# Kernel tuning notes

Hardware: AMD Instinct MI355X
Metric: run time of the kernel (lower is better)

## Reference

```python
import jax, jax.numpy as jnp
import numpy as np

K = 8  # hardcoded knn_point(8, ...) in the original module


def setup_inputs() -> dict:
    key = jax.random.key(0)
    k1, k2, k3 = jax.random.split(key, 3)
    B, N, S, C = 8, 8192, 2048, 256
    return {
        "xyz": jax.random.normal(k1, (B, 3, N), dtype=jnp.float32),
        "sparse_xyz": jax.random.normal(k2, (B, 3, S), dtype=jnp.float32),
        "sparse_feat": jax.random.normal(k3, (B, C, S), dtype=jnp.float32),
    }


def reference(xyz, sparse_xyz, sparse_feat):
    # xyz: [B,3,N] dense query points; sparse_xyz: [B,3,S]; sparse_feat: [B,C,S]
    B, _, N = xyz.shape
    x = jnp.transpose(xyz, (0, 2, 1))          # [B,N,3]
    sx = jnp.transpose(sparse_xyz, (0, 2, 1))  # [B,S,3]
    sf = jnp.transpose(sparse_feat, (0, 2, 1)) # [B,S,C]

    sqr = (jnp.sum(x * x, axis=-1)[:, :, None]
           + jnp.sum(sx * sx, axis=-1)[:, None, :]
           - 2.0 * jnp.einsum('bnc,bsc->bns', x, sx))

    # K nearest neighbors (smallest distance) -> indices [B,N,K]
    _, idx = jax.lax.top_k(-sqr, K)

    bidx = jnp.arange(B)[:, None, None]
    g_xyz = sx[bidx, idx]                      # gather neighbor coords [B,N,K,3]
    diff = g_xyz - x[:, :, None, :]
    dist = jnp.maximum(jnp.linalg.norm(diff, axis=3), 1e-10)  # [B,N,K]

    inv = 1.0 / dist
    weight = inv / jnp.sum(inv, axis=2, keepdims=True)        # [B,N,K]

    g_feat = sf[bidx, idx]                     # gather neighbor feats [B,N,K,C]
    dense = jnp.sum(weight[..., None] * g_feat, axis=2)       # [B,N,C]
    return jnp.transpose(dense, (0, 2, 1))     # [B,C,N]
```

## Files before the change

### kernel.cpp

```cpp
#include <hip/hip_runtime.h>
#include <hip/hip_fp16.h>

#define BB 8
#define NN 8192
#define SS 2048
#define CC 256
#define KNN 8
#define TOPM 10
#define NLIST 4
#define QPB 64
#define MSTRIDE 41
#define P2STR 66

#define UMIN(a, b) __builtin_elementwise_min(a, b)
#define UMAX(a, b) __builtin_elementwise_max(a, b)

typedef short bf16x8_t __attribute__((ext_vector_type(8)));
typedef float f32x4_t __attribute__((ext_vector_type(4)));

__device__ __forceinline__ float2 unpack_h2(unsigned u) {
    __half2 h = *reinterpret_cast<__half2*>(&u);
    return __half22float2(h);
}

__device__ __forceinline__ unsigned short f2bf(float f) {
    unsigned u = __float_as_uint(f);
    u += 0x7FFFu + ((u >> 16) & 1u);
    return (unsigned short)(u >> 16);
}
__device__ __forceinline__ float bf2f(unsigned short h) {
    return __uint_as_float((unsigned)h << 16);
}

__device__ __forceinline__ unsigned med3u(unsigned a, unsigned b, unsigned c) {
    unsigned d;
    asm("v_med3_u32 %0, %1, %2, %3" : "=v"(d) : "v"(a), "v"(b), "v"(c));
    return d;
}

__device__ __forceinline__ void ins1(unsigned k1[TOPM], unsigned c) {
#pragma unroll
    for (int j = TOPM - 1; j >= 1; --j)
        k1[j] = med3u(c, k1[j - 1], k1[j]);
    k1[0] = UMIN(k1[0], c);
}

__device__ __forceinline__ void ins_step(unsigned k1[TOPM], f32x4_t d, unsigned sbase) {
    ins1(k1, (__float_as_uint(d[0]) & 0xFFFFF800u) | sbase);
    ins1(k1, (__float_as_uint(d[1]) & 0xFFFFF800u) | (sbase + 1u));
    ins1(k1, (__float_as_uint(d[2]) & 0xFFFFF800u) | (sbase + 2u));
    ins1(k1, (__float_as_uint(d[3]) & 0xFFFFF800u) | (sbase + 3u));
}

__global__ __launch_bounds__(256) void prep_kernel(
    const float* __restrict__ sf,
    const float* __restrict__ sxyz,
    unsigned short* __restrict__ sft,
    unsigned short* __restrict__ gt)
{
    __shared__ unsigned short ts[64 * P2STR];

    const int blk = blockIdx.x;
    const int t   = threadIdx.x;

    if (blk < BB * 32 * 4) {
        const int b  = blk >> 7;
        const int st = (blk >> 2) & 31;
        const int c0 = (blk & 3) * 64;

        const int s  = t & 63;
        const int cq = t >> 6;
        const float* sfb = sf + ((long)b * CC + c0) * SS + st * 64;
#pragma unroll
        for (int it = 0; it < 16; ++it) {
            int c = it * 4 + cq;
            float v = sfb[(long)c * SS + s];
            ts[s * P2STR + c] = __half_as_ushort(__float2half_rn(v));
        }
        __syncthreads();

        const int so = t >> 2;
        const int cl = t & 3;
        const unsigned short* src = &ts[so * P2STR + cl * 16];
        unsigned u[8];
#pragma unroll
        for (int i = 0; i < 8; ++i) u[i] = *(const unsigned*)&src[i * 2];
        unsigned short* dst = sft + ((long)b * SS + st * 64 + so) * CC + c0 + cl * 16;
        *(uint4*)&dst[0] = make_uint4(u[0], u[1], u[2], u[3]);
        *(uint4*)&dst[8] = make_uint4(u[4], u[5], u[6], u[7]);
    } else {
        const int idx = blk - BB * 32 * 4;
        const int b = idx >> 3;
        const int s = (idx & 7) * 256 + t;
        const float* sb = sxyz + (long)b * 3 * SS;
        unsigned short* gb = gt + (long)b * 2 * SS * 8;

        float px = sb[s], py = sb[SS + s], pz = sb[2 * SS + s];
        unsigned short xh = f2bf(px); unsigned short xl = f2bf(px - bf2f(xh));
        unsigned short yh = f2bf(py); unsigned short yl = f2bf(py - bf2f(yh));
        unsigned short zh = f2bf(pz); unsigned short zl = f2bf(pz - bf2f(zh));
        float pn = fmaf(px, px, fmaf(py, py, pz * pz));
        unsigned short nh = f2bf(pn); unsigned short nl = f2bf(pn - bf2f(nh));
        const unsigned ONE = 0x3F80u;
        uint4 t0 = make_uint4((unsigned)xh | ((unsigned)xl << 16),
                              (unsigned)xh | ((unsigned)yh << 16),
                              (unsigned)yl | ((unsigned)yh << 16),
                              (unsigned)zh | ((unsigned)zl << 16));
        uint4 t1 = make_uint4((unsigned)zh | ((unsigned)nh << 16),
                              (unsigned)nl | (ONE << 16),
                              ONE, 0u);
        *(uint4*)&gb[(long)s * 8] = t0;
        *(uint4*)&gb[((long)SS + s) * 8] = t1;
    }
}

__global__ __launch_bounds__(256, 4) void knn_kernel(
    const float* __restrict__ xyz,
    const float* __restrict__ sxyz,
    const unsigned short* __restrict__ gt,
    const unsigned short* __restrict__ sft,
    float* __restrict__ out)
{
    __shared__ unsigned mbuf[QPB * MSTRIDE];
    __shared__ unsigned pk_lds[QPB * KNN];

    const int b    = blockIdx.x >> 7;
    const int q0   = (blockIdx.x & 127) * QPB;
    const int tid  = threadIdx.x;
    const int wave = tid >> 6;
    const int lane = tid & 63;
    const int g    = lane >> 4;
    const int qi   = lane & 15;

    const float* sb = sxyz + (long)b * 3 * SS;
    const float* xb = xyz + (long)b * 3 * NN;

    const int nq = q0 + wave * 16 + qi;
    const float qx = xb[nq], qy = xb[NN + nq], qz = xb[2 * NN + nq];

    bf16x8_t qf = (bf16x8_t)0;
    {
        unsigned short xh = f2bf(qx); float xhf = bf2f(xh);
        unsigned short yh = f2bf(qy); float yhf = bf2f(yh);
        unsigned short zh = f2bf(qz); float zhf = bf2f(zh);
        unsigned short xh2 = f2bf(-2.f * xhf), xl2 = f2bf(-2.f * (qx - xhf));
        unsigned short yh2 = f2bf(-2.f * yhf), yl2 = f2bf(-2.f * (qy - yhf));
        unsigned short zh2 = f2bf(-2.f * zhf), zl2 = f2bf(-2.f * (qz - zhf));
        float qn = fmaf(qx, qx, fmaf(qy, qy, qz * qz)) + 0.0625f;
        unsigned short nh = f2bf(qn); unsigned short nl = f2bf(qn - bf2f(nh));
        const short ONE = (short)0x3F80;
        if (g == 0) {
            qf[0] = (short)xh2; qf[1] = (short)xh2; qf[2] = (short)xl2;
            qf[3] = (short)yh2; qf[4] = (short)yh2; qf[5] = (short)yl2;
            qf[6] = (short)zh2; qf[7] = (short)zh2;
        } else if (g == 1) {
            qf[0] = (short)zl2; qf[1] = ONE; qf[2] = ONE;
            qf[3] = (short)nh;  qf[4] = (short)nl;
        }
    }

    const unsigned short* ap =
        gt + (long)b * 2 * SS * 8 + (long)(g & 1) * SS * 8 + qi * 8;

    unsigned k1[TOPM];
#pragma unroll
    for (int j = 0; j < TOPM; ++j) k1[j] = 0xFFFFFFFFu;

    const f32x4_t zacc = {0.f, 0.f, 0.f, 0.f};
    const unsigned ib4 = (unsigned)(g * 4);

    bf16x8_t a0 = *(const bf16x8_t*)ap; ap += 128;
    bf16x8_t a1 = *(const bf16x8_t*)ap; ap += 128;

    for (int step = 0; step < 126; step += 2) {
        f32x4_t d0 = __builtin_amdgcn_mfma_f32_16x16x32_bf16(a0, qf, zacc, 0, 0, 0);
        a0 = *(const bf16x8_t*)ap; ap += 128;
        ins_step(k1, d0, ib4 + (unsigned)(step * 16));
        f32x4_t d1 = __builtin_amdgcn_mfma_f32_16x16x32_bf16(a1, qf, zacc, 0, 0, 0);
        a1 = *(const bf16x8_t*)ap; ap += 128;
        ins_step(k1, d1, ib4 + (unsigned)((step + 1) * 16));
    }
    {
        f32x4_t d0 = __builtin_amdgcn_mfma_f32_16x16x32_bf16(a0, qf, zacc, 0, 0, 0);
        ins_step(k1, d0, ib4 + (unsigned)(126 * 16));
        f32x4_t d1 = __builtin_amdgcn_mfma_f32_16x16x32_bf16(a1, qf, zacc, 0, 0, 0);
        ins_step(k1, d1, ib4 + (unsigned)(127 * 16));
    }

    {
        unsigned* m1 = &mbuf[(wave * 16 + qi) * MSTRIDE + g * TOPM];
#pragma unroll
        for (int j = 0; j < TOPM; ++j) m1[j] = k1[j];
    }
    __syncthreads();

    if (tid < QPB) {
        const int n2 = q0 + tid;
        const double dqx = (double)xb[n2], dqy = (double)xb[NN + n2], dqz = (double)xb[2 * NN + n2];
        const unsigned* ml = &mbuf[tid * MSTRIDE];

        unsigned long long top[KNN];
#pragma unroll
        for (int j = 0; j < KNN; ++j) top[j] = ~0ull;

#pragma unroll 4
        for (int j = 0; j < NLIST * TOPM; ++j) {
            unsigned key = ml[j];
            int s = key & 0x7FF;
            float px = sb[s], py = sb[SS + s], pz = sb[2 * SS + s];
            double ex = (double)px - dqx;
            double ey = (double)py - dqy;
            double ez = (double)pz - dqz;
            double dd = ex * ex + ey * ey + ez * ez;
            unsigned long long c =
                (((unsigned long long)__double_as_longlong(dd)) & ~0x7FFull) | (unsigned long long)s;
#pragma unroll
            for (int jj = KNN - 1; jj >= 1; --jj)
                top[jj] = UMIN(UMAX(top[jj - 1], c), top[jj]);
            top[0] = UMIN(top[0], c);
        }

        const float fqx = xb[n2], fqy = xb[NN + n2], fqz = xb[2 * NN + n2];
        int   id[KNN];
        float inv[KNN];
        float ssum = 0.f;
#pragma unroll
        for (int k = 0; k < KNN; ++k) {
            id[k] = (int)(top[k] & 0x7FFull);
            float px = sb[id[k]], py = sb[SS + id[k]], pz = sb[2 * SS + id[k]];
            float dx = px - fqx, dy = py - fqy, dz = pz - fqz;
            float dv = sqrtf(dx * dx + dy * dy + dz * dz);
            dv = fmaxf(dv, 1e-10f);
            inv[k] = 1.0f / dv;
            ssum += inv[k];
        }
        const float rs = 1.0f / ssum;
#pragma unroll
        for (int k = 0; k < KNN; ++k) {
            unsigned hw = (unsigned)__half_as_ushort(__float2half_rn(inv[k] * rs));
            pk_lds[tid * KNN + k] = (hw << 16) | (unsigned)id[k];
        }
    }
    __syncthreads();

    {
        const int q  = tid >> 2;
        const int cl = tid & 3;
        const unsigned short* sfb = sft + (long)b * SS * CC;
        float* outq = out + (long)b * CC * NN + (q0 + q);

        unsigned pks[KNN];
#pragma unroll
        for (int k = 0; k < KNN; ++k) pks[k] = pk_lds[q * KNN + k];

#pragma unroll
        for (int cc = 0; cc < 8; ++cc) {
            const int ch = cc * 32 + cl * 8;
            float acc[8];
#pragma unroll
            for (int j = 0; j < 8; ++j) acc[j] = 0.f;

#pragma unroll
            for (int k = 0; k < KNN; ++k) {
                const unsigned p = pks[k];
                const int idp = p & 0x7FF;
                const float w = __half2float(__ushort_as_half((unsigned short)(p >> 16)));
                const uint4 F = *(const uint4*)&sfb[(long)idp * CC + ch];
                float2 f0 = unpack_h2(F.x), f1 = unpack_h2(F.y);
                float2 f2 = unpack_h2(F.z), f3 = unpack_h2(F.w);
                acc[0] = fmaf(w, f0.x, acc[0]);
                acc[1] = fmaf(w, f0.y, acc[1]);
                acc[2] = fmaf(w, f1.x, acc[2]);
                acc[3] = fmaf(w, f1.y, acc[3]);
                acc[4] = fmaf(w, f2.x, acc[4]);
                acc[5] = fmaf(w, f2.y, acc[5]);
                acc[6] = fmaf(w, f3.x, acc[6]);
                acc[7] = fmaf(w, f3.y, acc[7]);
            }
#pragma unroll
            for (int j = 0; j < 8; ++j)
                outq[(long)(ch + j) * NN] = acc[j];
        }
    }
}

extern "C" void kernel_launch(void* const* d_in, const int* in_sizes, int n_in,
                              void* d_out, int out_size, void* d_ws, size_t ws_size,
                              hipStream_t stream) {
    const float* xyz  = (const float*)d_in[0];
    const float* sxyz = (const float*)d_in[1];
    const float* sf   = (const float*)d_in[2];
    float* out = (float*)d_out;

    unsigned short* gtile = (unsigned short*)d_ws;
    unsigned short* sft   = (unsigned short*)((char*)d_ws + 512 * 1024);

    prep_kernel<<<dim3(BB * 32 * 4 + 64), dim3(256), 0, stream>>>(sf, sxyz, sft, gtile);
    knn_kernel<<<dim3(BB * NN / QPB), dim3(256), 0, stream>>>(xyz, sxyz, gtile, sft, out);
}
```

Measured before the change: 165.0 us.

## Split KNN scan across waves by sparse half, two query tiles per wave

Each wave now processes two 16-query tiles against half of the sparse points, instead of one tile against all of them. Each loaded A fragment of sparse coordinates is reused for two MFMAs, and the candidate merge list per query doubles to 8 sublists of 10. This halves global loads of the sparse-point fragments per MFMA and gives more independent insert chains for ILP. The cost is twice the top-M register state, a larger LDS buffer, and twice the candidates to rescore in the serial final selection by 64 threads.

```diff
diff --git a/kernel.cpp b/kernel.cpp
--- a/kernel.cpp
+++ b/kernel.cpp
@@ -7,9 +7,9 @@
 #define CC 256
 #define KNN 8
 #define TOPM 10
-#define NLIST 4
+#define NLIST 8
 #define QPB 64
-#define MSTRIDE 41
+#define MSTRIDE 81
 #define P2STR 66
 
 #define UMIN(a, b) __builtin_elementwise_min(a, b)
@@ -50,6 +50,29 @@
     ins1(k1, (__float_as_uint(d[1]) & 0xFFFFF800u) | (sbase + 1u));
     ins1(k1, (__float_as_uint(d[2]) & 0xFFFFF800u) | (sbase + 2u));
     ins1(k1, (__float_as_uint(d[3]) & 0xFFFFF800u) | (sbase + 3u));
+}
+
+__device__ __forceinline__ bf16x8_t make_qf(const float* xb, int n, int g) {
+    const float qx = xb[n], qy = xb[NN + n], qz = xb[2 * NN + n];
+    bf16x8_t qf = (bf16x8_t)0;
+    unsigned short xh = f2bf(qx); float xhf = bf2f(xh);
+    unsigned short yh = f2bf(qy); float yhf = bf2f(yh);
+    unsigned short zh = f2bf(qz); float zhf = bf2f(zh);
+    unsigned short xh2 = f2bf(-2.f * xhf), xl2 = f2bf(-2.f * (qx - xhf));
+    unsigned short yh2 = f2bf(-2.f * yhf), yl2 = f2bf(-2.f * (qy - yhf));
+    unsigned short zh2 = f2bf(-2.f * zhf), zl2 = f2bf(-2.f * (qz - zhf));
+    float qn = fmaf(qx, qx, fmaf(qy, qy, qz * qz)) + 0.0625f;
+    unsigned short nh = f2bf(qn); unsigned short nl = f2bf(qn - bf2f(nh));
+    const short ONE = (short)0x3F80;
+    if (g == 0) {
+        qf[0] = (short)xh2; qf[1] = (short)xh2; qf[2] = (short)xl2;
+        qf[3] = (short)yh2; qf[4] = (short)yh2; qf[5] = (short)yl2;
+        qf[6] = (short)zh2; qf[7] = (short)zh2;
+    } else if (g == 1) {
+        qf[0] = (short)zl2; qf[1] = ONE; qf[2] = ONE;
+        qf[3] = (short)nh;  qf[4] = (short)nl;
+    }
+    return qf;
 }
 
 __global__ __launch_bounds__(256) void prep_kernel(
@@ -131,66 +154,57 @@
     const int lane = tid & 63;
     const int g    = lane >> 4;
     const int qi   = lane & 15;
+    const int p    = wave & 1;
+    const int h    = wave >> 1;
 
     const float* sb = sxyz + (long)b * 3 * SS;
     const float* xb = xyz + (long)b * 3 * NN;
 
-    const int nq = q0 + wave * 16 + qi;
-    const float qx = xb[nq], qy = xb[NN + nq], qz = xb[2 * NN + nq];
-
-    bf16x8_t qf = (bf16x8_t)0;
-    {
-        unsigned short xh = f2bf(qx); float xhf = bf2f(xh);
-        unsigned short yh = f2bf(qy); float yhf = bf2f(yh);
-        unsigned short zh = f2bf(qz); float zhf = bf2f(zh);
-        unsigned short xh2 = f2bf(-2.f * xhf), xl2 = f2bf(-2.f * (qx - xhf));
-        unsigned short yh2 = f2bf(-2.f * yhf), yl2 = f2bf(-2.f * (qy - yhf));
-        unsigned short zh2 = f2bf(-2.f * zhf), zl2 = f2bf(-2.f * (qz - zhf));
-        float qn = fmaf(qx, qx, fmaf(qy, qy, qz * qz)) + 0.0625f;
-        unsigned short nh = f2bf(qn); unsigned short nl = f2bf(qn - bf2f(nh));
-        const short ONE = (short)0x3F80;
-        if (g == 0) {
-            qf[0] = (short)xh2; qf[1] = (short)xh2; qf[2] = (short)xl2;
-            qf[3] = (short)yh2; qf[4] = (short)yh2; qf[5] = (short)yl2;
-            qf[6] = (short)zh2; qf[7] = (short)zh2;
-        } else if (g == 1) {
-            qf[0] = (short)zl2; qf[1] = ONE; qf[2] = ONE;
-            qf[3] = (short)nh;  qf[4] = (short)nl;
-        }
-    }
+    const int nqA = q0 + p * 32 + qi;
+    const bf16x8_t qfA = make_qf(xb, nqA, g);
+    const bf16x8_t qfB = make_qf(xb, nqA + 16, g);
 
     const unsigned short* ap =
-        gt + (long)b * 2 * SS * 8 + (long)(g & 1) * SS * 8 + qi * 8;
-
-    unsigned k1[TOPM];
-#pragma unroll
-    for (int j = 0; j < TOPM; ++j) k1[j] = 0xFFFFFFFFu;
+        gt + (long)b * 2 * SS * 8 + (long)(g & 1) * SS * 8 + (long)h * 1024 * 8 + qi * 8;
+
+    unsigned k1A[TOPM], k1B[TOPM];
+#pragma unroll
+    for (int j = 0; j < TOPM; ++j) { k1A[j] = 0xFFFFFFFFu; k1B[j] = 0xFFFFFFFFu; }
 
     const f32x4_t zacc = {0.f, 0.f, 0.f, 0.f};
-    const unsigned ib4 = (unsigned)(g * 4);
+    const unsigned ib = (unsigned)(g * 4 + h * 1024);
 
     bf16x8_t a0 = *(const bf16x8_t*)ap; ap += 128;
     bf16x8_t a1 = *(const bf16x8_t*)ap; ap += 128;
 
-    for (int step = 0; step < 126; step += 2) {
-        f32x4_t d0 = __builtin_amdgcn_mfma_f32_16x16x32_bf16(a0, qf, zacc, 0, 0, 0);
+    for (int step = 0; step < 62; step += 2) {
+        f32x4_t d0 = __builtin_amdgcn_mfma_f32_16x16x32_bf16(a0, qfA, zacc, 0, 0, 0);
+        f32x4_t e0 = __builtin_amdgcn_mfma_f32_16x16x32_bf16(a0, qfB, zacc, 0, 0, 0);
         a0 = *(const bf16x8_t*)ap; ap += 128;
-        ins_step(k1, d0, ib4 + (unsigned)(step * 16));
-        f32x4_t d1 = __builtin_amdgcn_mfma_f32_16x16x32_bf16(a1, qf, zacc, 0, 0, 0);
+        ins_step(k1A, d0, ib + (unsigned)(step * 16));
+        ins_step(k1B, e0, ib + (unsigned)(step * 16));
+        f32x4_t d1 = __builtin_amdgcn_mfma_f32_16x16x32_bf16(a1, qfA, zacc, 0, 0, 0);
+        f32x4_t e1 = __builtin_amdgcn_mfma_f32_16x16x32_bf16(a1, qfB, zacc, 0, 0, 0);
         a1 = *(const bf16x8_t*)ap; ap += 128;
-        ins_step(k1, d1, ib4 + (unsigned)((step + 1) * 16));
+        ins_step(k1A, d1, ib + (unsigned)((step + 1) * 16));
+        ins_step(k1B, e1, ib + (unsigned)((step + 1) * 16));
     }
     {
-        f32x4_t d0 = __builtin_amdgcn_mfma_f32_16x16x32_bf16(a0, qf, zacc, 0, 0, 0);
-        ins_step(k1, d0, ib4 + (unsigned)(126 * 16));
-        f32x4_t d1 = __builtin_amdgcn_mfma_f32_16x16x32_bf16(a1, qf, zacc, 0, 0, 0);
-        ins_step(k1, d1, ib4 + (unsigned)(127 * 16));
+        f32x4_t d0 = __builtin_amdgcn_mfma_f32_16x16x32_bf16(a0, qfA, zacc, 0, 0, 0);
+        f32x4_t e0 = __builtin_amdgcn_mfma_f32_16x16x32_bf16(a0, qfB, zacc, 0, 0, 0);
+        ins_step(k1A, d0, ib + (unsigned)(62 * 16));
+        ins_step(k1B, e0, ib + (unsigned)(62 * 16));
+        f32x4_t d1 = __builtin_amdgcn_mfma_f32_16x16x32_bf16(a1, qfA, zacc, 0, 0, 0);
+        f32x4_t e1 = __builtin_amdgcn_mfma_f32_16x16x32_bf16(a1, qfB, zacc, 0, 0, 0);
+        ins_step(k1A, d1, ib + (unsigned)(63 * 16));
+        ins_step(k1B, e1, ib + (unsigned)(63 * 16));
     }
 
     {
-        unsigned* m1 = &mbuf[(wave * 16 + qi) * MSTRIDE + g * TOPM];
-#pragma unroll
-        for (int j = 0; j < TOPM; ++j) m1[j] = k1[j];
+        unsigned* mA = &mbuf[(p * 32 + qi) * MSTRIDE + (h * 4 + g) * TOPM];
+        unsigned* mB = &mbuf[(p * 32 + 16 + qi) * MSTRIDE + (h * 4 + g) * TOPM];
+#pragma unroll
+        for (int j = 0; j < TOPM; ++j) { mA[j] = k1A[j]; mB[j] = k1B[j]; }
     }
     __syncthreads();
 
@@ -262,9 +276,9 @@
 
 #pragma unroll
             for (int k = 0; k < KNN; ++k) {
-                const unsigned p = pks[k];
-                const int idp = p & 0x7FF;
-                const float w = __half2float(__ushort_as_half((unsigned short)(p >> 16)));
+                const unsigned p2 = pks[k];
+                const int idp = p2 & 0x7FF;
+                const float w = __half2float(__ushort_as_half((unsigned short)(p2 >> 16)));
                 const uint4 F = *(const uint4*)&sfb[(long)idp * CC + ch];
                 float2 f0 = unpack_h2(F.x), f1 = unpack_h2(F.y);
                 float2 f2 = unpack_h2(F.z), f3 = unpack_h2(F.w);
```

Result: slower. 170.6 us (+3.4%).
